# Performance work log

Measured on AMD Instinct MI355X. Metric: run time of the kernel, lower is better.

Reference implementation:

```python
import jax, jax.numpy as jnp
import numpy as np

B, H, W, C_IN, F = 4, 64, 64, 128, 256


def setup_inputs() -> dict:
    key = jax.random.key(0)
    ks = jax.random.split(key, 6)
    return {
        "inputs": jax.random.normal(ks[0], (B, H, W, C_IN), dtype=jnp.float32),
        "W_proj": jax.random.normal(ks[1], (C_IN, F), dtype=jnp.float32) * 0.02,
        "b_proj": jnp.zeros((F,), dtype=jnp.float32),
        "W_q": jax.random.normal(ks[2], (F, F), dtype=jnp.float32) * 0.02,
        "b_q": jnp.zeros((F,), dtype=jnp.float32),
        "W_k": jax.random.normal(ks[3], (F, F), dtype=jnp.float32) * 0.02,
        "b_k": jnp.zeros((F,), dtype=jnp.float32),
        "W_v": jax.random.normal(ks[4], (F, F), dtype=jnp.float32) * 0.02,
        "b_v": jnp.zeros((F,), dtype=jnp.float32),
        "gamma": jax.random.uniform(ks[5], (1,), dtype=jnp.float32),
    }


def reference(inputs, W_proj, b_proj, W_q, b_q, W_k, b_k, W_v, b_v, gamma):
    # 1x1 conv projection (C_in -> filters) since input channels != filters
    x = jnp.einsum("bhwc,cf->bhwf", inputs, W_proj) + b_proj  # [B,H,W,F]
    q = jnp.einsum("bhwf,fg->bhwg", x, W_q) + b_q
    k = jnp.einsum("bhwf,fg->bhwg", x, W_k) + b_k
    v = jnp.einsum("bhwf,fg->bhwg", x, W_v) + b_v
    b, h, w, f = x.shape
    n = h * w
    qr = q.reshape(b, n, f)
    kr = k.reshape(b, n, f)
    vr = v.reshape(b, n, f)
    attn = jax.nn.softmax(jnp.einsum("bnf,bmf->bnm", qr, kr), axis=-1)  # [B,N,N]
    context = jnp.einsum("bnm,bmf->bnf", attn, vr).reshape(b, h, w, f)
    return gamma * context + x
```

## Files before the change

### kernel.cpp

```cpp
#include <hip/hip_runtime.h>
#include <hip/hip_bf16.h>
#include <stdint.h>

typedef __attribute__((ext_vector_type(8))) short short8;
typedef __attribute__((ext_vector_type(4))) float floatx4;
typedef __attribute__((ext_vector_type(16))) float floatx16;

#define DEVI __device__ __forceinline__
#define MFMA16(a, b, c) __builtin_amdgcn_mfma_f32_16x16x32_bf16((a), (b), (c), 0, 0, 0)
#define MFMA32(a, b, c) __builtin_amdgcn_mfma_f32_32x32x16_fp8_fp8((a), (b), (c), 0, 0, 0)

typedef __attribute__((address_space(3))) unsigned int lds_u32;
typedef __attribute__((address_space(1))) const unsigned int glb_u32;
#define GLOAD_LDS16(g, l) __builtin_amdgcn_global_load_lds((glb_u32*)(g), (lds_u32*)(l), 16, 0, 0)

DEVI unsigned short f2bf(float x) {
    union { float f; unsigned int u; } v; v.f = x;
    unsigned int r = v.u + 0x7FFFu + ((v.u >> 16) & 1u);
    return (unsigned short)(r >> 16);
}
DEVI float bf2f(unsigned short h) {
    union { unsigned int u; float f; } v; v.u = ((unsigned int)h) << 16;
    return v.f;
}
DEVI unsigned char f2fp8(float x) {
    int c = __builtin_amdgcn_cvt_pk_fp8_f32(x, x, 0, false);
    return (unsigned char)(c & 0xFF);
}


__global__ void cast_f32_bf16(const float* __restrict__ in, unsigned short* __restrict__ out, int n4) {
    int i = blockIdx.x * blockDim.x + threadIdx.x;
    if (i < n4) {
        float4 v = ((const float4*)in)[i];
        ushort4 o;
        o.x = f2bf(v.x); o.y = f2bf(v.y); o.z = f2bf(v.z); o.w = f2bf(v.w);
        ((ushort4*)out)[i] = o;
    }
}

__global__ void transpose_cast(const float* __restrict__ W, unsigned short* __restrict__ Wt, int K, int N) {
    int idx = blockIdx.x * blockDim.x + threadIdx.x;
    if (idx < K * N) {
        int k = idx / N, n = idx % N;
        Wt[n * K + k] = f2bf(W[idx]);
    }
}

__global__ __launch_bounds__(256) void pack_k8(unsigned char* __restrict__ kb) {
    __shared__ unsigned char T[64][272];
    const int b = blockIdx.y, blk = blockIdx.x;
    unsigned char* base = kb + (size_t)b * 1048576 + (size_t)blk * 16384;
    const int tid = threadIdx.x;
    #pragma unroll
    for (int it = 0; it < 4; ++it) {
        int idx = tid + it * 256;
        int row = idx >> 4, col = (idx & 15) * 16;
        *(int4*)&T[row][col] = *(const int4*)&base[(size_t)row * 256 + col];
    }
    __syncthreads();
    const int w = tid >> 6, lane = tid & 63, l31 = lane & 31, hi = lane >> 5;
    const int tile = w >> 1, sh = (w & 1) * 8;
    #pragma unroll
    for (int i = 0; i < 8; ++i) {
        int s = sh + i;
        long o = *(const long*)&T[tile * 32 + l31][s * 16 + hi * 8];
        *(long*)&base[(size_t)tile * 8192 + (size_t)s * 512 + lane * 8] = o;
    }
}

__global__ __launch_bounds__(256) void pack_v8(unsigned char* __restrict__ vb) {
    __shared__ unsigned char T[64][272];
    const int b = blockIdx.y, blk = blockIdx.x;
    unsigned char* base = vb + (size_t)b * 1048576 + (size_t)blk * 16384;
    const int tid = threadIdx.x;
    #pragma unroll
    for (int it = 0; it < 4; ++it) {
        int idx = tid + it * 256;
        int row = idx >> 4, col = (idx & 15) * 16;
        *(int4*)&T[row][col] = *(const int4*)&base[(size_t)row * 256 + col];
    }
    __syncthreads();
    const int w = tid >> 6, lane = tid & 63, l31 = lane & 31, hi = lane >> 5;
    const int tile = w >> 1, hw = w & 1;
    #pragma unroll
    for (int i = 0; i < 8; ++i) {
        int c = hw * 8 + i;
        int fb = c >> 1, s2 = c & 1;
        union { unsigned char bts[8]; long l; } o;
        #pragma unroll
        for (int j = 0; j < 8; ++j)
            o.bts[j] = T[tile * 32 + s2 * 16 + hi * 8 + j][fb * 32 + l31];
        *(long*)&base[(size_t)tile * 8192 + (size_t)c * 512 + lane * 8] = o.l;
    }
}


template<int K>
__global__ __launch_bounds__(256) void gemm_bias(
    const unsigned short* __restrict__ A,
    const unsigned short* __restrict__ Wt,
    const float* __restrict__ bias,
    unsigned short* __restrict__ Cb,
    int M, int N)
{
    __shared__ unsigned short As[64][136];
    __shared__ unsigned short Bs[64][136];
    const int tid  = threadIdx.x;
    const int w    = tid >> 6;
    const int lane = tid & 63;
    const int quad = lane >> 4;
    const int l15  = lane & 15;
    const int m0 = blockIdx.x * 64;
    const int n0 = blockIdx.y * 64;

    floatx4 acc[4];
    #pragma unroll
    for (int t = 0; t < 4; ++t) acc[t] = (floatx4)0.0f;

    for (int kc = 0; kc < K; kc += 128) {
        __syncthreads();
        #pragma unroll
        for (int idx = tid; idx < 1024; idx += 256) {
            int r = idx >> 4, g = idx & 15;
            *(short8*)&As[r][g * 8] = *(const short8*)&A[(size_t)(m0 + r) * K + kc + g * 8];
            *(short8*)&Bs[r][g * 8] = *(const short8*)&Wt[(size_t)(n0 + r) * K + kc + g * 8];
        }
        __syncthreads();
        #pragma unroll
        for (int s = 0; s < 4; ++s) {
            short8 a = *(const short8*)&As[w * 16 + l15][s * 32 + quad * 8];
            #pragma unroll
            for (int t = 0; t < 4; ++t) {
                short8 bfr = *(const short8*)&Bs[t * 16 + l15][s * 32 + quad * 8];
                acc[t] = MFMA16(a, bfr, acc[t]);
            }
        }
    }

    #pragma unroll
    for (int t = 0; t < 4; ++t) {
        int n = n0 + t * 16 + l15;
        float bs = bias[n];
        #pragma unroll
        for (int r = 0; r < 4; ++r) {
            int m = m0 + w * 16 + quad * 4 + r;
            Cb[(size_t)m * N + n] = f2bf(acc[t][r] + bs);
        }
    }
}

__global__ __launch_bounds__(256) void gemm_qkv(
    const unsigned short* __restrict__ A,
    const unsigned short* __restrict__ Wt0, const unsigned short* __restrict__ Wt1, const unsigned short* __restrict__ Wt2,
    const float* __restrict__ b0, const float* __restrict__ b1, const float* __restrict__ b2,
    unsigned char* __restrict__ C0, unsigned char* __restrict__ C1, unsigned char* __restrict__ C2,
    int M, int N)
{
    const unsigned short* Wt = (blockIdx.z == 0) ? Wt0 : (blockIdx.z == 1) ? Wt1 : Wt2;
    const float* bias        = (blockIdx.z == 0) ? b0  : (blockIdx.z == 1) ? b1  : b2;
    unsigned char* Cb        = (blockIdx.z == 0) ? C0  : (blockIdx.z == 1) ? C1  : C2;

    __shared__ unsigned short As[64][136];
    __shared__ unsigned short Bs[64][136];
    const int tid  = threadIdx.x;
    const int w    = tid >> 6;
    const int lane = tid & 63;
    const int quad = lane >> 4;
    const int l15  = lane & 15;
    const int m0 = blockIdx.x * 64;
    const int n0 = blockIdx.y * 64;

    floatx4 acc[4];
    #pragma unroll
    for (int t = 0; t < 4; ++t) acc[t] = (floatx4)0.0f;

    for (int kc = 0; kc < 256; kc += 128) {
        __syncthreads();
        #pragma unroll
        for (int idx = tid; idx < 1024; idx += 256) {
            int r = idx >> 4, g = idx & 15;
            *(short8*)&As[r][g * 8] = *(const short8*)&A[(size_t)(m0 + r) * 256 + kc + g * 8];
            *(short8*)&Bs[r][g * 8] = *(const short8*)&Wt[(size_t)(n0 + r) * 256 + kc + g * 8];
        }
        __syncthreads();
        #pragma unroll
        for (int s = 0; s < 4; ++s) {
            short8 a = *(const short8*)&As[w * 16 + l15][s * 32 + quad * 8];
            #pragma unroll
            for (int t = 0; t < 4; ++t) {
                short8 bfr = *(const short8*)&Bs[t * 16 + l15][s * 32 + quad * 8];
                acc[t] = MFMA16(a, bfr, acc[t]);
            }
        }
    }

    #pragma unroll
    for (int t = 0; t < 4; ++t) {
        int n = n0 + t * 16 + l15;
        float bs = bias[n];
        #pragma unroll
        for (int r = 0; r < 4; ++r) {
            int m = m0 + w * 16 + quad * 4 + r;
            Cb[(size_t)m * N + n] = f2fp8(acc[t][r] + bs);
        }
    }
}


__global__ __launch_bounds__(512, 2) void flash_attn(
    const unsigned char* __restrict__ qg,
    const unsigned char* __restrict__ kp,
    const unsigned char* __restrict__ vp,
    const unsigned short* __restrict__ xb,
    const float* __restrict__ gamma,
    float* __restrict__ out)
{
    __shared__ __align__(16) unsigned char KV[2][65536];
    float* MbF = (float*)&KV[0][0];
    float* Ml  = MbF + 64 * 264;

    const int tid  = threadIdx.x;
    const int w    = tid >> 6;
    const int lane = tid & 63;
    const int l31  = lane & 31;
    const int hi   = lane >> 5;
    const int kq   = w & 3;
    const int rw   = w >> 2;
    const int blk  = blockIdx.x;
    const int b    = (blk & 7) >> 1;
    const int rt   = (blk >> 3) * 2 + (blk & 1);
    const int row0 = rt * 64 + rw * 32;

    const size_t baseQ = ((size_t)b * 4096 + row0 + l31) * 256 + hi * 8;
    long qf[16];
    #pragma unroll
    for (int s = 0; s < 16; ++s)
        qf[s] = *(const long*)&qg[baseQ + s * 16];

    const long ones8 = 0x3838383838383838L;

    floatx16 ctx[8];
    #pragma unroll
    for (int i = 0; i < 8; ++i) ctx[i] = (floatx16)0.0f;
    floatx16 lacc = (floatx16)0.0f;

    const unsigned char* kb_b = kp + (size_t)b * 1048576;
    const unsigned char* vb_b = vp + (size_t)b * 1048576;

#define FA_STAGE(T, BUF)                                                             \
    {                                                                                \
        _Pragma("unroll")                                                            \
        for (int p = 0; p < 8; ++p) {                                                \
            const int c    = p * 8 + w;                                              \
            const int ckq  = c >> 4;                                                 \
            const int csel = (c >> 3) & 1;                                           \
            const int coff = (c & 7) * 1024;                                         \
            const unsigned char* src = (csel ? vb_b : kb_b)                          \
                + (size_t)ckq * 262144 + (size_t)(T) * 8192 + coff + lane * 16;      \
            GLOAD_LDS16(src, &KV[BUF][ckq * 16384 + csel * 8192 + coff]);            \
        }                                                                            \
    }

    FA_STAGE(0, 0)

    for (int t = 0; t < 32; ++t) {
        const int buf = t & 1;
        __syncthreads();
        if (t < 31) FA_STAGE(t + 1, buf ^ 1)

        const unsigned char* kc = &KV[buf][kq * 16384];
        const unsigned char* vc = &KV[buf][kq * 16384 + 8192];

        floatx16 sa = (floatx16)0.0f, sb = (floatx16)0.0f;
        #pragma unroll
        for (int s = 0; s < 16; s += 2) {
            long k0 = *(const long*)&kc[(size_t)s * 512 + lane * 8];
            long k1 = *(const long*)&kc[(size_t)(s + 1) * 512 + lane * 8];
            sa = MFMA32(k0, qf[s], sa);
            sb = MFMA32(k1, qf[s + 1], sb);
        }

        float e[16];
        #pragma unroll
        for (int r = 0; r < 16; ++r) e[r] = __expf(sa[r] + sb[r]);
        int X0 = __builtin_amdgcn_cvt_pk_fp8_f32(e[0],  e[1],  0,  false);
        X0     = __builtin_amdgcn_cvt_pk_fp8_f32(e[2],  e[3],  X0, true);
        int Y0 = __builtin_amdgcn_cvt_pk_fp8_f32(e[4],  e[5],  0,  false);
        Y0     = __builtin_amdgcn_cvt_pk_fp8_f32(e[6],  e[7],  Y0, true);
        int X1 = __builtin_amdgcn_cvt_pk_fp8_f32(e[8],  e[9],  0,  false);
        X1     = __builtin_amdgcn_cvt_pk_fp8_f32(e[10], e[11], X1, true);
        int Y1 = __builtin_amdgcn_cvt_pk_fp8_f32(e[12], e[13], 0,  false);
        Y1     = __builtin_amdgcn_cvt_pk_fp8_f32(e[14], e[15], Y1, true);
        asm volatile("v_permlane32_swap_b32 %0, %1" : "+v"(X0), "+v"(Y0));
        asm volatile("v_permlane32_swap_b32 %0, %1" : "+v"(X1), "+v"(Y1));
        union { int i2[2]; long l; } u0, u1;
        u0.i2[0] = X0; u0.i2[1] = Y0;
        u1.i2[0] = X1; u1.i2[1] = Y1;
        const long ap0 = u0.l;
        const long ap1 = u1.l;

        lacc = MFMA32(ap0, ones8, lacc);
        lacc = MFMA32(ap1, ones8, lacc);
        #pragma unroll
        for (int fb = 0; fb < 8; ++fb) {
            long v0 = *(const long*)&vc[(size_t)(fb * 2)     * 512 + lane * 8];
            long v1 = *(const long*)&vc[(size_t)(fb * 2 + 1) * 512 + lane * 8];
            ctx[fb] = MFMA32(ap0, v0, ctx[fb]);
            ctx[fb] = MFMA32(ap1, v1, ctx[fb]);
        }
    }
#undef FA_STAGE

    __syncthreads();
    for (int pass = 3; pass >= 0; --pass) {
        if (kq == pass) {
            #pragma unroll
            for (int fb = 0; fb < 8; ++fb) {
                #pragma unroll
                for (int r = 0; r < 16; ++r) {
                    int row = rw * 32 + (r & 3) + 8 * (r >> 2) + 4 * hi;
                    int idx = row * 264 + fb * 32 + l31;
                    float prev = (pass == 3) ? 0.0f : MbF[idx];
                    MbF[idx] = prev + ctx[fb][r];
                }
            }
            if (l31 == 0) {
                #pragma unroll
                for (int r = 0; r < 16; ++r) {
                    int row = rw * 32 + (r & 3) + 8 * (r >> 2) + 4 * hi;
                    float prev = (pass == 3) ? 0.0f : Ml[row];
                    Ml[row] = prev + lacc[r];
                }
            }
        }
        __syncthreads();
    }

    const float g = gamma[0];
    const int row = tid >> 3;
    const int c0  = (tid & 7) * 32;
    const float rl = 1.0f / Ml[row];
    const size_t o = ((size_t)b * 4096 + rt * 64 + row) * 256 + c0;
    #pragma unroll
    for (int j = 0; j < 4; ++j) {
        short8 xv = *(const short8*)&xb[o + j * 8];
        float res[8];
        #pragma unroll
        for (int i = 0; i < 8; ++i)
            res[i] = g * MbF[row * 264 + c0 + j * 8 + i] * rl + bf2f((unsigned short)xv[i]);
        *(float4*)&out[o + j * 8]     = *(float4*)&res[0];
        *(float4*)&out[o + j * 8 + 4] = *(float4*)&res[4];
    }
}


extern "C" void kernel_launch(void* const* d_in, const int* in_sizes, int n_in,
                              void* d_out, int out_size, void* d_ws, size_t ws_size,
                              hipStream_t stream)
{
    const float* inp   = (const float*)d_in[0];
    const float* Wp    = (const float*)d_in[1];
    const float* bp    = (const float*)d_in[2];
    const float* Wq    = (const float*)d_in[3];
    const float* bq    = (const float*)d_in[4];
    const float* Wk    = (const float*)d_in[5];
    const float* bk    = (const float*)d_in[6];
    const float* Wv    = (const float*)d_in[7];
    const float* bv    = (const float*)d_in[8];
    const float* gamma = (const float*)d_in[9];
    float* out = (float*)d_out;

    char* ws = (char*)d_ws;
    unsigned char*  q8    = (unsigned char*)(ws + 0);
    unsigned char*  k8    = (unsigned char*)(ws + 4194304);
    unsigned char*  v8    = (unsigned char*)(ws + 8388608);
    unsigned short* x_b   = (unsigned short*)(ws + 12582912);
    unsigned short* in_b  = (unsigned short*)(ws + 20971520);
    unsigned short* Wt_p  = (unsigned short*)(ws + 25165824);
    unsigned short* Wt_q  = (unsigned short*)(ws + 25231360);
    unsigned short* Wt_k  = (unsigned short*)(ws + 25362432);
    unsigned short* Wt_v  = (unsigned short*)(ws + 25493504);

    cast_f32_bf16<<<2048, 256, 0, stream>>>(inp, in_b, 2097152 / 4);
    transpose_cast<<<128, 256, 0, stream>>>(Wp, Wt_p, 128, 256);
    transpose_cast<<<256, 256, 0, stream>>>(Wq, Wt_q, 256, 256);
    transpose_cast<<<256, 256, 0, stream>>>(Wk, Wt_k, 256, 256);
    transpose_cast<<<256, 256, 0, stream>>>(Wv, Wt_v, 256, 256);

    gemm_bias<128><<<dim3(256, 4), 256, 0, stream>>>(in_b, Wt_p, bp, x_b, 16384, 256);
    gemm_qkv<<<dim3(256, 4, 3), 256, 0, stream>>>(x_b, Wt_q, Wt_k, Wt_v, bq, bk, bv,
                                                  q8, k8, v8, 16384, 256);
    pack_k8<<<dim3(64, 4), 256, 0, stream>>>(k8);
    pack_v8<<<dim3(64, 4), 256, 0, stream>>>(v8);

    flash_attn<<<256, 512, 0, stream>>>(q8, k8, v8, x_b, gamma, out);
}
```

Measured before the change: 206.7 us.

## Fuse input cast, weight prep and K/V packing into GEMM kernels; widen attention loads

The fp32-to-bf16 input cast moves into the projection GEMM, the four weight transposes merge into one launch, and the separate K/V fp8 pack kernels become part of the QKV GEMM epilogue, which writes the MFMA-friendly layout through LDS. GEMM outputs are staged through LDS so global stores are 16-byte coalesced. The attention inner loop now uses 16-byte K/V loads and raises wave priority around its MFMA bursts. This removes several launches and intermediate round trips through global memory, at the cost of extra LDS traffic and a new interleaved 16-byte K/V layout that the attention loads must match.

```diff
diff --git a/kernel.cpp b/kernel.cpp
--- a/kernel.cpp
+++ b/kernel.cpp
@@ -5,6 +5,7 @@
 typedef __attribute__((ext_vector_type(8))) short short8;
 typedef __attribute__((ext_vector_type(4))) float floatx4;
 typedef __attribute__((ext_vector_type(16))) float floatx16;
+typedef __attribute__((ext_vector_type(2))) long longx2;
 
 #define DEVI __device__ __forceinline__
 #define MFMA16(a, b, c) __builtin_amdgcn_mfma_f32_16x16x32_bf16((a), (b), (c), 0, 0, 0)
@@ -28,84 +29,36 @@
     return (unsigned char)(c & 0xFF);
 }
 
-
-__global__ void cast_f32_bf16(const float* __restrict__ in, unsigned short* __restrict__ out, int n4) {
-    int i = blockIdx.x * blockDim.x + threadIdx.x;
-    if (i < n4) {
-        float4 v = ((const float4*)in)[i];
-        ushort4 o;
-        o.x = f2bf(v.x); o.y = f2bf(v.y); o.z = f2bf(v.z); o.w = f2bf(v.w);
-        ((ushort4*)out)[i] = o;
-    }
-}
-
-__global__ void transpose_cast(const float* __restrict__ W, unsigned short* __restrict__ Wt, int K, int N) {
+__global__ __launch_bounds__(256) void prep_weights(
+    const float* __restrict__ Wp, const float* __restrict__ Wq,
+    const float* __restrict__ Wk, const float* __restrict__ Wv,
+    unsigned short* __restrict__ Tp, unsigned short* __restrict__ Tq,
+    unsigned short* __restrict__ Tk, unsigned short* __restrict__ Tv)
+{
     int idx = blockIdx.x * blockDim.x + threadIdx.x;
-    if (idx < K * N) {
-        int k = idx / N, n = idx % N;
-        Wt[n * K + k] = f2bf(W[idx]);
-    }
-}
-
-__global__ __launch_bounds__(256) void pack_k8(unsigned char* __restrict__ kb) {
-    __shared__ unsigned char T[64][272];
-    const int b = blockIdx.y, blk = blockIdx.x;
-    unsigned char* base = kb + (size_t)b * 1048576 + (size_t)blk * 16384;
-    const int tid = threadIdx.x;
-    #pragma unroll
-    for (int it = 0; it < 4; ++it) {
-        int idx = tid + it * 256;
-        int row = idx >> 4, col = (idx & 15) * 16;
-        *(int4*)&T[row][col] = *(const int4*)&base[(size_t)row * 256 + col];
-    }
-    __syncthreads();
-    const int w = tid >> 6, lane = tid & 63, l31 = lane & 31, hi = lane >> 5;
-    const int tile = w >> 1, sh = (w & 1) * 8;
-    #pragma unroll
-    for (int i = 0; i < 8; ++i) {
-        int s = sh + i;
-        long o = *(const long*)&T[tile * 32 + l31][s * 16 + hi * 8];
-        *(long*)&base[(size_t)tile * 8192 + (size_t)s * 512 + lane * 8] = o;
-    }
-}
-
-__global__ __launch_bounds__(256) void pack_v8(unsigned char* __restrict__ vb) {
-    __shared__ unsigned char T[64][272];
-    const int b = blockIdx.y, blk = blockIdx.x;
-    unsigned char* base = vb + (size_t)b * 1048576 + (size_t)blk * 16384;
-    const int tid = threadIdx.x;
-    #pragma unroll
-    for (int it = 0; it < 4; ++it) {
-        int idx = tid + it * 256;
-        int row = idx >> 4, col = (idx & 15) * 16;
-        *(int4*)&T[row][col] = *(const int4*)&base[(size_t)row * 256 + col];
-    }
-    __syncthreads();
-    const int w = tid >> 6, lane = tid & 63, l31 = lane & 31, hi = lane >> 5;
-    const int tile = w >> 1, hw = w & 1;
-    #pragma unroll
-    for (int i = 0; i < 8; ++i) {
-        int c = hw * 8 + i;
-        int fb = c >> 1, s2 = c & 1;
-        union { unsigned char bts[8]; long l; } o;
-        #pragma unroll
-        for (int j = 0; j < 8; ++j)
-            o.bts[j] = T[tile * 32 + s2 * 16 + hi * 8 + j][fb * 32 + l31];
-        *(long*)&base[(size_t)tile * 8192 + (size_t)c * 512 + lane * 8] = o.l;
-    }
-}
-
-
-template<int K>
+    if (idx < 32768) {
+        int k = idx >> 8, n = idx & 255;
+        Tp[n * 128 + k] = f2bf(Wp[idx]);
+    } else {
+        int r = idx - 32768;
+        int m = r >> 16, i = r & 65535;
+        const float* W   = (m == 0) ? Wq : (m == 1) ? Wk : Wv;
+        unsigned short* T = (m == 0) ? Tq : (m == 1) ? Tk : Tv;
+        int k = i >> 8, n = i & 255;
+        T[n * 256 + k] = f2bf(W[i]);
+    }
+}
+
+
 __global__ __launch_bounds__(256) void gemm_bias(
-    const unsigned short* __restrict__ A,
+    const float* __restrict__ A,
     const unsigned short* __restrict__ Wt,
     const float* __restrict__ bias,
     unsigned short* __restrict__ Cb,
-    int M, int N)
-{
-    __shared__ unsigned short As[64][136];
-    __shared__ unsigned short Bs[64][136];
+    int N)
+{
+    __shared__ __align__(16) unsigned short As[64][136];
+    __shared__ __align__(16) unsigned short Bs[64][136];
     const int tid  = threadIdx.x;
     const int w    = tid >> 6;
     const int lane = tid & 63;
@@ -118,13 +71,84 @@
     #pragma unroll
     for (int t = 0; t < 4; ++t) acc[t] = (floatx4)0.0f;
 
-    for (int kc = 0; kc < K; kc += 128) {
+    #pragma unroll
+    for (int it = 0; it < 8; ++it) {
+        int idx = tid + it * 256;
+        int r = idx >> 5, c4 = idx & 31;
+        float4 v = *(const float4*)&A[(size_t)(m0 + r) * 128 + c4 * 4];
+        ushort4 o;
+        o.x = f2bf(v.x); o.y = f2bf(v.y); o.z = f2bf(v.z); o.w = f2bf(v.w);
+        *(ushort4*)&As[r][c4 * 4] = o;
+    }
+    #pragma unroll
+    for (int it = 0; it < 4; ++it) {
+        int idx = tid + it * 256;
+        int r = idx >> 4, g = idx & 15;
+        *(short8*)&Bs[r][g * 8] = *(const short8*)&Wt[(size_t)(n0 + r) * 128 + g * 8];
+    }
+    __syncthreads();
+    #pragma unroll
+    for (int s = 0; s < 4; ++s) {
+        short8 a = *(const short8*)&As[w * 16 + l15][s * 32 + quad * 8];
+        #pragma unroll
+        for (int t = 0; t < 4; ++t) {
+            short8 bfr = *(const short8*)&Bs[t * 16 + l15][s * 32 + quad * 8];
+            acc[t] = MFMA16(a, bfr, acc[t]);
+        }
+    }
+
+    __syncthreads();
+    unsigned short* T = &As[0][0];
+    #pragma unroll
+    for (int t = 0; t < 4; ++t) {
+        int n = n0 + t * 16 + l15;
+        float bs = bias[n];
+        #pragma unroll
+        for (int r = 0; r < 4; ++r)
+            T[(w * 16 + quad * 4 + r) * 80 + t * 16 + l15] = f2bf(acc[t][r] + bs);
+    }
+    __syncthreads();
+    int row = tid >> 2, c8 = (tid & 3) * 8;
+    #pragma unroll
+    for (int half = 0; half < 2; ++half) {
+        int4 ov = *(const int4*)&T[row * 80 + c8 + half * 32];
+        *(int4*)&Cb[(size_t)(m0 + row) * N + n0 + c8 + half * 32] = ov;
+    }
+}
+
+
+__global__ __launch_bounds__(256) void gemm_qkv(
+    const unsigned short* __restrict__ A,
+    const unsigned short* __restrict__ Wt0, const unsigned short* __restrict__ Wt1, const unsigned short* __restrict__ Wt2,
+    const float* __restrict__ b0, const float* __restrict__ b1, const float* __restrict__ b2,
+    unsigned char* __restrict__ C0, unsigned char* __restrict__ C1, unsigned char* __restrict__ C2,
+    int N)
+{
+    const unsigned short* Wt = (blockIdx.z == 0) ? Wt0 : (blockIdx.z == 1) ? Wt1 : Wt2;
+    const float* bias        = (blockIdx.z == 0) ? b0  : (blockIdx.z == 1) ? b1  : b2;
+    unsigned char* Cb        = (blockIdx.z == 0) ? C0  : (blockIdx.z == 1) ? C1  : C2;
+
+    __shared__ __align__(16) unsigned short As[64][136];
+    __shared__ __align__(16) unsigned short Bs[64][136];
+    const int tid  = threadIdx.x;
+    const int w    = tid >> 6;
+    const int lane = tid & 63;
+    const int quad = lane >> 4;
+    const int l15  = lane & 15;
+    const int m0 = blockIdx.x * 64;
+    const int n0 = blockIdx.y * 64;
+
+    floatx4 acc[4];
+    #pragma unroll
+    for (int t = 0; t < 4; ++t) acc[t] = (floatx4)0.0f;
+
+    for (int kc = 0; kc < 256; kc += 128) {
         __syncthreads();
         #pragma unroll
         for (int idx = tid; idx < 1024; idx += 256) {
             int r = idx >> 4, g = idx & 15;
-            *(short8*)&As[r][g * 8] = *(const short8*)&A[(size_t)(m0 + r) * K + kc + g * 8];
-            *(short8*)&Bs[r][g * 8] = *(const short8*)&Wt[(size_t)(n0 + r) * K + kc + g * 8];
+            *(short8*)&As[r][g * 8] = *(const short8*)&A[(size_t)(m0 + r) * 256 + kc + g * 8];
+            *(short8*)&Bs[r][g * 8] = *(const short8*)&Wt[(size_t)(n0 + r) * 256 + kc + g * 8];
         }
         __syncthreads();
         #pragma unroll
@@ -138,72 +162,45 @@
         }
     }
 
+    __syncthreads();
+    unsigned char* T = (unsigned char*)&As[0][0];
     #pragma unroll
     for (int t = 0; t < 4; ++t) {
         int n = n0 + t * 16 + l15;
         float bs = bias[n];
         #pragma unroll
-        for (int r = 0; r < 4; ++r) {
-            int m = m0 + w * 16 + quad * 4 + r;
-            Cb[(size_t)m * N + n] = f2bf(acc[t][r] + bs);
-        }
-    }
-}
-
-__global__ __launch_bounds__(256) void gemm_qkv(
-    const unsigned short* __restrict__ A,
-    const unsigned short* __restrict__ Wt0, const unsigned short* __restrict__ Wt1, const unsigned short* __restrict__ Wt2,
-    const float* __restrict__ b0, const float* __restrict__ b1, const float* __restrict__ b2,
-    unsigned char* __restrict__ C0, unsigned char* __restrict__ C1, unsigned char* __restrict__ C2,
-    int M, int N)
-{
-    const unsigned short* Wt = (blockIdx.z == 0) ? Wt0 : (blockIdx.z == 1) ? Wt1 : Wt2;
-    const float* bias        = (blockIdx.z == 0) ? b0  : (blockIdx.z == 1) ? b1  : b2;
-    unsigned char* Cb        = (blockIdx.z == 0) ? C0  : (blockIdx.z == 1) ? C1  : C2;
-
-    __shared__ unsigned short As[64][136];
-    __shared__ unsigned short Bs[64][136];
-    const int tid  = threadIdx.x;
-    const int w    = tid >> 6;
-    const int lane = tid & 63;
-    const int quad = lane >> 4;
-    const int l15  = lane & 15;
-    const int m0 = blockIdx.x * 64;
-    const int n0 = blockIdx.y * 64;
-
-    floatx4 acc[4];
-    #pragma unroll
-    for (int t = 0; t < 4; ++t) acc[t] = (floatx4)0.0f;
-
-    for (int kc = 0; kc < 256; kc += 128) {
-        __syncthreads();
-        #pragma unroll
-        for (int idx = tid; idx < 1024; idx += 256) {
-            int r = idx >> 4, g = idx & 15;
-            *(short8*)&As[r][g * 8] = *(const short8*)&A[(size_t)(m0 + r) * 256 + kc + g * 8];
-            *(short8*)&Bs[r][g * 8] = *(const short8*)&Wt[(size_t)(n0 + r) * 256 + kc + g * 8];
-        }
-        __syncthreads();
-        #pragma unroll
-        for (int s = 0; s < 4; ++s) {
-            short8 a = *(const short8*)&As[w * 16 + l15][s * 32 + quad * 8];
+        for (int r = 0; r < 4; ++r)
+            T[(w * 16 + quad * 4 + r) * 80 + t * 16 + l15] = f2fp8(acc[t][r] + bs);
+    }
+    __syncthreads();
+
+    const int b  = m0 >> 12;
+    const int mt = (m0 & 4095) >> 5;
+
+    if (blockIdx.z == 0) {
+        int row = tid >> 2, c16 = (tid & 3) * 16;
+        int4 vq = *(const int4*)&T[row * 80 + c16];
+        *(int4*)&Cb[(size_t)(m0 + row) * 256 + n0 + c16] = vq;
+    } else {
+        const int kt  = tid >> 7;
+        const int sub = (tid >> 6) & 1;
+        const int ln  = tid & 63;
+        const int l31b = ln & 31, hib = ln >> 5;
+        union { long h[2]; int4 v; unsigned char bts[16]; } o;
+        if (blockIdx.z == 1) {
             #pragma unroll
-            for (int t = 0; t < 4; ++t) {
-                short8 bfr = *(const short8*)&Bs[t * 16 + l15][s * 32 + quad * 8];
-                acc[t] = MFMA16(a, bfr, acc[t]);
-            }
-        }
-    }
-
-    #pragma unroll
-    for (int t = 0; t < 4; ++t) {
-        int n = n0 + t * 16 + l15;
-        float bs = bias[n];
-        #pragma unroll
-        for (int r = 0; r < 4; ++r) {
-            int m = m0 + w * 16 + quad * 4 + r;
-            Cb[(size_t)m * N + n] = f2fp8(acc[t][r] + bs);
-        }
+            for (int h = 0; h < 2; ++h)
+                o.h[h] = *(const long*)&T[(kt * 32 + l31b) * 80 + (sub * 2 + h) * 16 + hib * 8];
+        } else {
+            #pragma unroll
+            for (int s2 = 0; s2 < 2; ++s2)
+                #pragma unroll
+                for (int j = 0; j < 8; ++j)
+                    o.bts[s2 * 8 + j] = T[(kt * 32 + s2 * 16 + hib * 8 + j) * 80 + sub * 32 + l31b];
+        }
+        unsigned char* dst = Cb + (size_t)b * 1048576 + (size_t)(mt + kt) * 8192
+                           + (size_t)((n0 >> 5) + sub) * 1024 + ln * 16;
+        *(int4*)dst = o.v;
     }
 }
 
@@ -272,14 +269,18 @@
         const unsigned char* kc = &KV[buf][kq * 16384];
         const unsigned char* vc = &KV[buf][kq * 16384 + 8192];
 
+        longx2 kk[8];
+        #pragma unroll
+        for (int p = 0; p < 8; ++p)
+            kk[p] = *(const longx2*)&kc[p * 1024 + lane * 16];
         floatx16 sa = (floatx16)0.0f, sb = (floatx16)0.0f;
-        #pragma unroll
-        for (int s = 0; s < 16; s += 2) {
-            long k0 = *(const long*)&kc[(size_t)s * 512 + lane * 8];
-            long k1 = *(const long*)&kc[(size_t)(s + 1) * 512 + lane * 8];
-            sa = MFMA32(k0, qf[s], sa);
-            sb = MFMA32(k1, qf[s + 1], sb);
-        }
+        __builtin_amdgcn_s_setprio(1);
+        #pragma unroll
+        for (int p = 0; p < 8; ++p) {
+            sa = MFMA32(kk[p].x, qf[2 * p],     sa);
+            sb = MFMA32(kk[p].y, qf[2 * p + 1], sb);
+        }
+        __builtin_amdgcn_s_setprio(0);
 
         float e[16];
         #pragma unroll
@@ -302,13 +303,14 @@
 
         lacc = MFMA32(ap0, ones8, lacc);
         lacc = MFMA32(ap1, ones8, lacc);
-        #pragma unroll
-        for (int fb = 0; fb < 8; ++fb) {
-            long v0 = *(const long*)&vc[(size_t)(fb * 2)     * 512 + lane * 8];
-            long v1 = *(const long*)&vc[(size_t)(fb * 2 + 1) * 512 + lane * 8];
-            ctx[fb] = MFMA32(ap0, v0, ctx[fb]);
-            ctx[fb] = MFMA32(ap1, v1, ctx[fb]);
-        }
+        __builtin_amdgcn_s_setprio(1);
+        #pragma unroll
+        for (int p = 0; p < 8; ++p) {
+            longx2 vv = *(const longx2*)&vc[p * 1024 + lane * 16];
+            ctx[p] = MFMA32(ap0, vv.x, ctx[p]);
+            ctx[p] = MFMA32(ap1, vv.y, ctx[p]);
+        }
+        __builtin_amdgcn_s_setprio(0);
     }
 #undef FA_STAGE
 
@@ -376,23 +378,14 @@
     unsigned char*  k8    = (unsigned char*)(ws + 4194304);
     unsigned char*  v8    = (unsigned char*)(ws + 8388608);
     unsigned short* x_b   = (unsigned short*)(ws + 12582912);
-    unsigned short* in_b  = (unsigned short*)(ws + 20971520);
-    unsigned short* Wt_p  = (unsigned short*)(ws + 25165824);
-    unsigned short* Wt_q  = (unsigned short*)(ws + 25231360);
-    unsigned short* Wt_k  = (unsigned short*)(ws + 25362432);
-    unsigned short* Wt_v  = (unsigned short*)(ws + 25493504);
-
-    cast_f32_bf16<<<2048, 256, 0, stream>>>(inp, in_b, 2097152 / 4);
-    transpose_cast<<<128, 256, 0, stream>>>(Wp, Wt_p, 128, 256);
-    transpose_cast<<<256, 256, 0, stream>>>(Wq, Wt_q, 256, 256);
-    transpose_cast<<<256, 256, 0, stream>>>(Wk, Wt_k, 256, 256);
-    transpose_cast<<<256, 256, 0, stream>>>(Wv, Wt_v, 256, 256);
-
-    gemm_bias<128><<<dim3(256, 4), 256, 0, stream>>>(in_b, Wt_p, bp, x_b, 16384, 256);
+    unsigned short* Wt_p  = (unsigned short*)(ws + 20971520);
+    unsigned short* Wt_q  = (unsigned short*)(ws + 21037056);
+    unsigned short* Wt_k  = (unsigned short*)(ws + 21168128);
+    unsigned short* Wt_v  = (unsigned short*)(ws + 21299200);
+
+    prep_weights<<<896, 256, 0, stream>>>(Wp, Wq, Wk, Wv, Wt_p, Wt_q, Wt_k, Wt_v);
+    gemm_bias<<<dim3(256, 4), 256, 0, stream>>>(inp, Wt_p, bp, x_b, 256);
     gemm_qkv<<<dim3(256, 4, 3), 256, 0, stream>>>(x_b, Wt_q, Wt_k, Wt_v, bq, bk, bv,
-                                                  q8, k8, v8, 16384, 256);
-    pack_k8<<<dim3(64, 4), 256, 0, stream>>>(k8);
-    pack_v8<<<dim3(64, 4), 256, 0, stream>>>(v8);
-
+                                                  q8, k8, v8, 256);
     flash_attn<<<256, 512, 0, stream>>>(q8, k8, v8, x_b, gamma, out);
 }
```

New measurement: 190.4 us (median of 2 runs). 1.09x faster.
